# Performance work log

Hardware: AMD Instinct MI355X
Metric: run time of the kernel (lower is better)

The kernel has to match this reference:

```python
import jax, jax.numpy as jnp
import numpy as np

N, E, G = 50000, 800000, 200
F_IN, C, HEADS = 16, 64, 4
HID = C * HEADS  # 256


def setup_inputs() -> dict:
    key = jax.random.key(0)
    ks = jax.random.split(key, 30)
    rn = lambda k, s, sc=0.1: jax.random.normal(k, s, jnp.float32) * sc
    inp = {
        'x': jax.random.normal(ks[0], (N, F_IN), jnp.float32),
        'edge_index': jax.random.randint(ks[1], (2, E), 0, N, jnp.int32),
        'batch': jnp.sort(jax.random.randint(ks[2], (N,), 0, G, jnp.int32)),
        'Wl1': rn(ks[3], (F_IN, HID)), 'Wr1': rn(ks[4], (F_IN, HID)),
        'att1': rn(ks[5], (HEADS, C)), 'b1': rn(ks[6], (HID,)),
        'g1': jnp.ones((HID,), jnp.float32), 'be1': jnp.zeros((HID,), jnp.float32),
        'Wl2': rn(ks[7], (HID, HID)), 'Wr2': rn(ks[8], (HID, HID)),
        'att2': rn(ks[9], (HEADS, C)), 'b2': rn(ks[10], (HID,)),
        'g2': jnp.ones((HID,), jnp.float32), 'be2': jnp.zeros((HID,), jnp.float32),
        # GATv2 layer 3: 256 -> 64, 1 head, mean (concat=False)
        'Wl3': rn(ks[11], (HID, C)), 'Wr3': rn(ks[12], (HID, C)),
        'att3': rn(ks[13], (1, C)), 'b3': rn(ks[14], (C,)),
        'g3': jnp.ones((C,), jnp.float32), 'be3': jnp.zeros((C,), jnp.float32),
        # classifier MLP: 128 -> 64 -> 1
        'Wc1': rn(ks[15], (2 * C, C)), 'bc1': rn(ks[16], (C,)),
        'Wc2': rn(ks[17], (C, 1)), 'bc2': rn(ks[18], (1,)),
    }
    return inp


def _gatv2(x, src, dst, Wl, Wr, att, b, heads, c, concat):
    n = x.shape[0]
    xl = (x @ Wl).reshape(n, heads, c)
    xr = (x @ Wr).reshape(n, heads, c)
    s = jax.nn.leaky_relu(xl[src] + xr[dst], 0.2)       # [E', H, C]
    e = jnp.einsum('ehc,hc->eh', s, att)                 # [E', H]
    m = jax.ops.segment_max(e, dst, num_segments=n)
    p = jnp.exp(e - m[dst])
    denom = jax.ops.segment_sum(p, dst, num_segments=n)
    alpha = p / (denom[dst] + 1e-16)
    out = jax.ops.segment_sum(alpha[:, :, None] * xl[src], dst, num_segments=n)
    out = out.reshape(n, heads * c) if concat else out.mean(axis=1)
    return out + b


def _bn(x, g, b):
    mu = x.mean(0)
    v = x.var(0)
    return (x - mu) * jax.lax.rsqrt(v + 1e-5) * g + b


def reference(x, edge_index, batch,
              Wl1, Wr1, att1, b1, g1, be1,
              Wl2, Wr2, att2, b2, g2, be2,
              Wl3, Wr3, att3, b3, g3, be3,
              Wc1, bc1, Wc2, bc2):
    n = x.shape[0]
    loop = jnp.arange(n, dtype=edge_index.dtype)
    src = jnp.concatenate([edge_index[0], loop])  # PyG add_self_loops=True
    dst = jnp.concatenate([edge_index[1], loop])

    h = _gatv2(x, src, dst, Wl1, Wr1, att1, b1, HEADS, C, True)
    h = jax.nn.elu(_bn(h, g1, be1))  # dropout disabled (eval)
    h = _gatv2(h, src, dst, Wl2, Wr2, att2, b2, HEADS, C, True)
    h = jax.nn.elu(_bn(h, g2, be2))
    h = _gatv2(h, src, dst, Wl3, Wr3, att3, b3, 1, C, False)
    h = _bn(h, g3, be3)

    cnt = jax.ops.segment_sum(jnp.ones((n, 1), h.dtype), batch, num_segments=G)
    mean_pool = jax.ops.segment_sum(h, batch, num_segments=G) / jnp.maximum(cnt, 1.0)
    max_pool = jax.ops.segment_max(h, batch, num_segments=G)
    pooled = jnp.concatenate([mean_pool, max_pool], axis=1)  # [G, 128]

    out = jax.nn.relu(pooled @ Wc1 + bc1)
    out = out @ Wc2 + bc2  # [G, 1]
    return out
```

## Files before the change

### kernel.cpp

```cpp
#include <hip/hip_runtime.h>
#include <math.h>

#define N_NODES 50000
#define N_EDGES 800000
#define ET (N_EDGES + N_NODES)
#define N_GRAPHS 200
#define F_INN 16
#define C_DIM 64
#define N_HEADS 4
#define HIDD 256
#define SCAN_BLOCKS ((N_NODES + 255) / 256)

typedef __attribute__((ext_vector_type(8))) short short8;
typedef __attribute__((ext_vector_type(8))) ushort ushort8;
typedef __attribute__((ext_vector_type(4))) float f32x4;
typedef __attribute__((ext_vector_type(2))) float f32x2;

#define LOG2E 1.44269504088896340736f

__device__ __forceinline__ float bf2f(ushort u) {
  return __uint_as_float(((unsigned)u) << 16);
}
__device__ __forceinline__ ushort f2bf(float f) {
  unsigned u = __float_as_uint(f);
  u += 0x7fff + ((u >> 16) & 1);
  return (ushort)(u >> 16);
}
__device__ __forceinline__ float ex2(float x) {
#if __has_builtin(__builtin_amdgcn_exp2f)
  return __builtin_amdgcn_exp2f(x);
#else
  return exp2f(x);
#endif
}

__device__ __forceinline__ f32x2 emax2(f32x2 a, f32x2 b) {
#if __has_builtin(__builtin_elementwise_max)
  return __builtin_elementwise_max(a, b);
#else
  f32x2 r;
  r.x = fmaxf(a.x, b.x);
  r.y = fmaxf(a.y, b.y);
  return r;
#endif
}

template<int K, int M>
__global__ __launch_bounds__(256) void gemm_dual(
    const float* __restrict__ A, const float* __restrict__ Bl,
    const float* __restrict__ Br, ushort* __restrict__ Clb,
    ushort* __restrict__ Crb, int nrows)
{
  __shared__ __align__(16) float As[16][64];
  __shared__ __align__(16) float Bls[16][64];
  __shared__ __align__(16) float Brs[16][64];
  int tid = threadIdx.x;
  int row0 = blockIdx.x * 64;
  int col0 = blockIdx.y * 64;
  int tr = (tid >> 4) << 2;
  int tc = (tid & 15) << 2;
  float accL[4][4] = {{0.f}}, accR[4][4] = {{0.f}};
  int arow = tid >> 2, ak = (tid & 3) << 2;
  int brow = tid >> 4, bcol = (tid & 15) << 2;
  for (int k0 = 0; k0 < K; k0 += 16) {
    float4 av = make_float4(0.f, 0.f, 0.f, 0.f);
    int gr = row0 + arow;
    if (gr < nrows) av = *(const float4*)&A[(size_t)gr * K + k0 + ak];
    As[ak + 0][arow] = av.x;
    As[ak + 1][arow] = av.y;
    As[ak + 2][arow] = av.z;
    As[ak + 3][arow] = av.w;
    *(float4*)&Bls[brow][bcol] = *(const float4*)&Bl[(size_t)(k0 + brow) * M + col0 + bcol];
    *(float4*)&Brs[brow][bcol] = *(const float4*)&Br[(size_t)(k0 + brow) * M + col0 + bcol];
    __syncthreads();
    #pragma unroll
    for (int k = 0; k < 16; ++k) {
      float4 a = *(const float4*)&As[k][tr];
      float4 bl = *(const float4*)&Bls[k][tc];
      float4 br = *(const float4*)&Brs[k][tc];
      float aa[4] = {a.x, a.y, a.z, a.w};
      float lb[4] = {bl.x, bl.y, bl.z, bl.w};
      float rb[4] = {br.x, br.y, br.z, br.w};
      #pragma unroll
      for (int ii = 0; ii < 4; ++ii)
        #pragma unroll
        for (int jj = 0; jj < 4; ++jj) {
          accL[ii][jj] = fmaf(aa[ii], lb[jj], accL[ii][jj]);
          accR[ii][jj] = fmaf(aa[ii], rb[jj], accR[ii][jj]);
        }
    }
    __syncthreads();
  }
  #pragma unroll
  for (int ii = 0; ii < 4; ++ii) {
    int gr = row0 + tr + ii;
    if (gr < nrows) {
      *(ushort4*)&Clb[(size_t)gr * M + col0 + tc] =
          make_ushort4(f2bf(accL[ii][0]), f2bf(accL[ii][1]),
                       f2bf(accL[ii][2]), f2bf(accL[ii][3]));
      *(ushort4*)&Crb[(size_t)gr * M + col0 + tc] =
          make_ushort4(f2bf(accR[ii][0]), f2bf(accR[ii][1]),
                       f2bf(accR[ii][2]), f2bf(accR[ii][3]));
    }
  }
}

__device__ __forceinline__ void split_bf16(float a, ushort& hi, ushort& lo) {
  unsigned u = __float_as_uint(a);
  hi = (ushort)(u >> 16);
  float ah = __uint_as_float(u & 0xffff0000u);
  float r = a - ah;
  lo = (ushort)(__float_as_uint(r) >> 16);
}

template<int K, int N>
__global__ void convertB(const float* __restrict__ W, ushort* __restrict__ BTmat) {
  int idx = blockIdx.x * blockDim.x + threadIdx.x;
  if (idx >= K * N) return;
  int k = idx / N, n = idx - k * N;
  ushort hi, lo;
  split_bf16(W[idx], hi, lo);
  size_t dst = ((size_t)(k >> 3) * N + n) * 8 + (k & 7);
  BTmat[dst] = hi;
  BTmat[(size_t)(K / 8) * N * 8 + dst] = lo;
}

template<int N>
__global__ __launch_bounds__(N * 2) void gemm_fused(
    const float* __restrict__ H, const float* __restrict__ gsum,
    const float* __restrict__ gsumsq, const float* __restrict__ g,
    const float* __restrict__ be, const ushort* __restrict__ BT,
    ushort* __restrict__ Clb, ushort* __restrict__ Crb)
{
  constexpr int THREADS = N * 2;
  constexpr int PLANE = 32 * N * 8;
  __shared__ float SCs[256], SHs[256];
  __shared__ ushort Ah_s[32 * 256];
  __shared__ ushort Al_s[32 * 256];
  const int tid = threadIdx.x;
  const int brow0 = blockIdx.x * 32;

  const float invn = 1.0f / (float)N_NODES;
  for (int c = tid; c < 256; c += THREADS) {
    float mu = gsum[c] * invn;
    float var = gsumsq[c] * invn - mu * mu;
    float sc = g[c] * rsqrtf(var + 1e-5f);
    SCs[c] = sc;
    SHs[c] = be[c] - mu * sc;
  }
  __syncthreads();

  for (int gid = tid; gid < 1024; gid += THREADS) {
    int r = gid >> 5;
    int ch0 = (gid & 31) * 8;
    int grow = min(brow0 + r, N_NODES - 1);
    float4 v0 = *(const float4*)&H[(size_t)grow * 256 + ch0];
    float4 v1 = *(const float4*)&H[(size_t)grow * 256 + ch0 + 4];
    float4 sc0 = *(const float4*)&SCs[ch0];
    float4 sc1 = *(const float4*)&SCs[ch0 + 4];
    float4 sh0 = *(const float4*)&SHs[ch0];
    float4 sh1 = *(const float4*)&SHs[ch0 + 4];
    float vv[8] = {v0.x, v0.y, v0.z, v0.w, v1.x, v1.y, v1.z, v1.w};
    float scv[8] = {sc0.x, sc0.y, sc0.z, sc0.w, sc1.x, sc1.y, sc1.z, sc1.w};
    float shv[8] = {sh0.x, sh0.y, sh0.z, sh0.w, sh1.x, sh1.y, sh1.z, sh1.w};
    short8 hi8, lo8;
    #pragma unroll
    for (int j = 0; j < 8; ++j) {
      float t = fmaf(vv[j], scv[j], shv[j]);
      float e = t > 0.f ? t : __expf(t) - 1.f;
      ushort h, l;
      split_bf16(e, h, l);
      hi8[j] = (short)h;
      lo8[j] = (short)l;
    }
    int off = r * 512 + ((ch0 * 2) ^ ((r & 7) << 4));
    *(short8*)((char*)Ah_s + off) = hi8;
    *(short8*)((char*)Al_s + off) = lo8;
  }
  __syncthreads();

  const int wave = tid >> 6, lane = tid & 63;
  const int cn = lane & 15, kgrp = lane >> 4;
  const int combc = wave * 64;
  const bool isR = combc >= N;
  const ushort* Bh = BT + (isR ? 2 * PLANE : 0);
  const ushort* Bl_ = Bh + PLANE;
  const int cb = combc & (N - 1);
  f32x4 acc[2][4];
  #pragma unroll
  for (int rt = 0; rt < 2; ++rt)
    #pragma unroll
    for (int ct = 0; ct < 4; ++ct) acc[rt][ct] = (f32x4)(0.f);

  #pragma unroll 2
  for (int k0 = 0; k0 < 256; k0 += 32) {
    short8 ah[2], al[2];
    #pragma unroll
    for (int rt = 0; rt < 2; ++rt) {
      int row = rt * 16 + cn;
      int off = row * 512 + (((k0 * 2) + kgrp * 16) ^ ((row & 7) << 4));
      ah[rt] = *(const short8*)((const char*)Ah_s + off);
      al[rt] = *(const short8*)((const char*)Al_s + off);
    }
    const size_t bbase = (size_t)((k0 >> 3) + kgrp) * (N * 8);
    #pragma unroll
    for (int ct = 0; ct < 4; ++ct) {
      const size_t bo = bbase + (size_t)(cb + ct * 16 + cn) * 8;
      short8 bh = *(const short8*)&Bh[bo];
      short8 bl = *(const short8*)&Bl_[bo];
      #pragma unroll
      for (int rt = 0; rt < 2; ++rt) {
        acc[rt][ct] = __builtin_amdgcn_mfma_f32_16x16x32_bf16(ah[rt], bh, acc[rt][ct], 0, 0, 0);
        acc[rt][ct] = __builtin_amdgcn_mfma_f32_16x16x32_bf16(ah[rt], bl, acc[rt][ct], 0, 0, 0);
        acc[rt][ct] = __builtin_amdgcn_mfma_f32_16x16x32_bf16(al[rt], bh, acc[rt][ct], 0, 0, 0);
      }
    }
  }

  #pragma unroll
  for (int ct = 0; ct < 4; ++ct) {
    int cc = cb + ct * 16 + cn;
    #pragma unroll
    for (int rt = 0; rt < 2; ++rt) {
      int crow0 = brow0 + rt * 16 + kgrp * 4;
      #pragma unroll
      for (int j = 0; j < 4; ++j) {
        int rr = crow0 + j;
        if (rr < N_NODES) {
          if (!isR) Clb[(size_t)rr * N + cc] = f2bf(acc[rt][ct][j]);
          else      Crb[(size_t)rr * N + cc] = f2bf(acc[rt][ct][j]);
        }
      }
    }
  }
}

__global__ void hist_kernel(const int* __restrict__ dsts, int* __restrict__ curs) {
  int i = blockIdx.x * blockDim.x + threadIdx.x;
  if (i >= ET) return;
  int d = (i < N_EDGES) ? dsts[i] : i - N_EDGES;
  atomicAdd(&curs[d], 1);
}

__global__ __launch_bounds__(256) void scan_part(
    const int* __restrict__ curs, int* __restrict__ rows, int* __restrict__ bsum)
{
  __shared__ int tmp[256];
  int t = threadIdx.x;
  int i = blockIdx.x * 256 + t;
  int v = (i < N_NODES) ? curs[i] : 0;
  tmp[t] = v;
  __syncthreads();
  #pragma unroll
  for (int off = 1; off < 256; off <<= 1) {
    int u = (t >= off) ? tmp[t - off] : 0;
    __syncthreads();
    tmp[t] += u;
    __syncthreads();
  }
  if (i < N_NODES) rows[i] = tmp[t] - v;
  if (t == 255) bsum[blockIdx.x] = tmp[255];
}

__global__ __launch_bounds__(256) void scan_bsums(
    const int* __restrict__ bsum, int* __restrict__ boff)
{
  __shared__ int tmp[256];
  int t = threadIdx.x;
  int v = (t < SCAN_BLOCKS) ? bsum[t] : 0;
  tmp[t] = v;
  __syncthreads();
  #pragma unroll
  for (int off = 1; off < 256; off <<= 1) {
    int u = (t >= off) ? tmp[t - off] : 0;
    __syncthreads();
    tmp[t] += u;
    __syncthreads();
  }
  if (t < SCAN_BLOCKS) boff[t] = tmp[t] - v;
}

__global__ __launch_bounds__(256) void scan_apply(
    int* __restrict__ rows, const int* __restrict__ boff, int* __restrict__ curs)
{
  int i = blockIdx.x * 256 + threadIdx.x;
  if (i < N_NODES) {
    int r = rows[i] + boff[blockIdx.x];
    rows[i] = r;
    curs[i] = r;
  }
  if (i == 0) rows[N_NODES] = ET;
}

__global__ void scatter_kernel(const int* __restrict__ srcs, const int* __restrict__ dsts,
                               int* __restrict__ curs, int* __restrict__ esrc) {
  int i = blockIdx.x * blockDim.x + threadIdx.x;
  if (i >= ET) return;
  int s, d;
  if (i < N_EDGES) { s = srcs[i]; d = dsts[i]; } else { s = d = i - N_EDGES; }
  int pos = atomicAdd(&curs[d], 1);
  esrc[pos] = s;
}

__global__ __launch_bounds__(256) void flash256(
    const ushort* __restrict__ xl, const ushort* __restrict__ xr,
    const float* __restrict__ att, const int* __restrict__ rows,
    const int* __restrict__ esrc, float* __restrict__ out)
{
  const int wave = threadIdx.x >> 6, lane = threadIdx.x & 63;
  const int d = blockIdx.x * 4 + wave;
  const unsigned lo4 = lane * 4;
  int beg = rows[d], end = rows[d + 1];
  ushort4 ur = *(const ushort4*)&xr[(size_t)d * 256 + lo4];
  float xq0 = bf2f(ur.x), xq1 = bf2f(ur.y), xq2 = bf2f(ur.z), xq3 = bf2f(ur.w);
  float4 w = *(const float4*)&att[lo4];
  w.x *= LOG2E; w.y *= LOG2E; w.z *= LOG2E; w.w *= LOG2E;
  auto score = [&](float b0, float b1, float b2, float b3) {
    float v0 = b0 + xq0, v1 = b1 + xq1, v2 = b2 + xq2, v3 = b3 + xq3;
    v0 = v0 > 0.f ? v0 : 0.2f * v0;
    v1 = v1 > 0.f ? v1 : 0.2f * v1;
    v2 = v2 > 0.f ? v2 : 0.2f * v2;
    v3 = v3 > 0.f ? v3 : 0.2f * v3;
    return fmaf(v0, w.x, fmaf(v1, w.y, fmaf(v2, w.z, v3 * w.w)));
  };
  float m = -INFINITY, s = 0.f;
  float a0 = 0.f, a1 = 0.f, a2 = 0.f, a3 = 0.f;
  int p = beg;
  for (; p + 4 <= end; p += 4) {
    int s1 = esrc[p], s2 = esrc[p + 1], s3 = esrc[p + 2], s4 = esrc[p + 3];
    unsigned o1 = ((unsigned)s1 << 8) + lo4;
    unsigned o2 = ((unsigned)s2 << 8) + lo4;
    unsigned o3 = ((unsigned)s3 << 8) + lo4;
    unsigned o4 = ((unsigned)s4 << 8) + lo4;
    ushort4 u1 = *(const ushort4*)&xl[o1];
    ushort4 u2 = *(const ushort4*)&xl[o2];
    ushort4 u3 = *(const ushort4*)&xl[o3];
    ushort4 u4 = *(const ushort4*)&xl[o4];
    float b10 = bf2f(u1.x), b11 = bf2f(u1.y), b12 = bf2f(u1.z), b13 = bf2f(u1.w);
    float b20 = bf2f(u2.x), b21 = bf2f(u2.y), b22 = bf2f(u2.z), b23 = bf2f(u2.w);
    float b30 = bf2f(u3.x), b31 = bf2f(u3.y), b32 = bf2f(u3.z), b33 = bf2f(u3.w);
    float b40 = bf2f(u4.x), b41 = bf2f(u4.y), b42 = bf2f(u4.z), b43 = bf2f(u4.w);
    float e1 = score(b10, b11, b12, b13);
    float e2 = score(b20, b21, b22, b23);
    float e3 = score(b30, b31, b32, b33);
    float e4 = score(b40, b41, b42, b43);
    e1 += __shfl_xor(e1, 1); e2 += __shfl_xor(e2, 1);
    e3 += __shfl_xor(e3, 1); e4 += __shfl_xor(e4, 1);
    e1 += __shfl_xor(e1, 2); e2 += __shfl_xor(e2, 2);
    e3 += __shfl_xor(e3, 2); e4 += __shfl_xor(e4, 2);
    e1 += __shfl_xor(e1, 4); e2 += __shfl_xor(e2, 4);
    e3 += __shfl_xor(e3, 4); e4 += __shfl_xor(e4, 4);
    e1 += __shfl_xor(e1, 8); e2 += __shfl_xor(e2, 8);
    e3 += __shfl_xor(e3, 8); e4 += __shfl_xor(e4, 8);
    float gm = fmaxf(fmaxf(e1, e2), fmaxf(e3, e4));
    if (__all(gm <= m + 8.0f)) {
      float p1 = ex2(e1 - m);
      float p2 = ex2(e2 - m);
      float p3 = ex2(e3 - m);
      float p4 = ex2(e4 - m);
      s += (p1 + p2) + (p3 + p4);
      a0 = fmaf(p1, b10, fmaf(p2, b20, fmaf(p3, b30, fmaf(p4, b40, a0))));
      a1 = fmaf(p1, b11, fmaf(p2, b21, fmaf(p3, b31, fmaf(p4, b41, a1))));
      a2 = fmaf(p1, b12, fmaf(p2, b22, fmaf(p3, b32, fmaf(p4, b42, a2))));
      a3 = fmaf(p1, b13, fmaf(p2, b23, fmaf(p3, b33, fmaf(p4, b43, a3))));
    } else {
      float mn = fmaxf(m, gm);
      float f = ex2(m - mn);
      float p1 = ex2(e1 - mn);
      float p2 = ex2(e2 - mn);
      float p3 = ex2(e3 - mn);
      float p4 = ex2(e4 - mn);
      s = s * f + ((p1 + p2) + (p3 + p4));
      a0 = fmaf(a0, f, fmaf(p1, b10, fmaf(p2, b20, fmaf(p3, b30, p4 * b40))));
      a1 = fmaf(a1, f, fmaf(p1, b11, fmaf(p2, b21, fmaf(p3, b31, p4 * b41))));
      a2 = fmaf(a2, f, fmaf(p1, b12, fmaf(p2, b22, fmaf(p3, b32, p4 * b42))));
      a3 = fmaf(a3, f, fmaf(p1, b13, fmaf(p2, b23, fmaf(p3, b33, p4 * b43))));
      m = mn;
    }
  }
  for (; p < end; ++p) {
    int s1 = esrc[p];
    unsigned o1 = ((unsigned)s1 << 8) + lo4;
    ushort4 u1 = *(const ushort4*)&xl[o1];
    float b10 = bf2f(u1.x), b11 = bf2f(u1.y), b12 = bf2f(u1.z), b13 = bf2f(u1.w);
    float e1 = score(b10, b11, b12, b13);
    e1 += __shfl_xor(e1, 1);
    e1 += __shfl_xor(e1, 2);
    e1 += __shfl_xor(e1, 4);
    e1 += __shfl_xor(e1, 8);
    float mn = fmaxf(m, e1);
    float f = ex2(m - mn);
    float p1 = ex2(e1 - mn);
    s = fmaf(s, f, p1);
    a0 = fmaf(a0, f, p1 * b10);
    a1 = fmaf(a1, f, p1 * b11);
    a2 = fmaf(a2, f, p1 * b12);
    a3 = fmaf(a3, f, p1 * b13);
    m = mn;
  }
  float inv = 1.f / (s + 1e-16f);
  *(float4*)&out[(size_t)d * 256 + lo4] =
      make_float4(a0 * inv, a1 * inv, a2 * inv, a3 * inv);
}

__global__ __launch_bounds__(256) void flash64(
    const ushort* __restrict__ xl, const ushort* __restrict__ xr,
    const float* __restrict__ att, const int* __restrict__ rows,
    const int* __restrict__ esrc, float* __restrict__ out)
{
  const int wave = threadIdx.x >> 6, lane = threadIdx.x & 63;
  const int di = lane >> 3, sl = lane & 7;
  const int idx = blockIdx.x * 32 + wave * 8 + di;
  const bool valid = idx < N_NODES;
  const int d = valid ? idx : N_NODES - 1;
  const unsigned ch = sl * 8;
  ushort8 uxr = *(const ushort8*)&xr[(size_t)d * 64 + ch];
  float4 wa = *(const float4*)&att[ch];
  float4 wb = *(const float4*)&att[ch + 4];
  f32x2 xr0 = {bf2f(uxr[0]), bf2f(uxr[1])}, xr1 = {bf2f(uxr[2]), bf2f(uxr[3])};
  f32x2 xr2 = {bf2f(uxr[4]), bf2f(uxr[5])}, xr3 = {bf2f(uxr[6]), bf2f(uxr[7])};
  f32x2 w0 = {wa.x * LOG2E, wa.y * LOG2E}, w1 = {wa.z * LOG2E, wa.w * LOG2E};
  f32x2 w2 = {wb.x * LOG2E, wb.y * LOG2E}, w3 = {wb.z * LOG2E, wb.w * LOG2E};
  int beg = rows[d], end = rows[d + 1];
  float m = -INFINITY, s = 0.f;
  f32x2 a0 = {0.f, 0.f}, a1 = {0.f, 0.f}, a2 = {0.f, 0.f}, a3 = {0.f, 0.f};

  auto loadb = [&](int src, f32x2 b[4]) {
    unsigned off = ((unsigned)src << 6) + ch;
    ushort8 u = *(const ushort8*)&xl[off];
    b[0] = f32x2{bf2f(u[0]), bf2f(u[1])};
    b[1] = f32x2{bf2f(u[2]), bf2f(u[3])};
    b[2] = f32x2{bf2f(u[4]), bf2f(u[5])};
    b[3] = f32x2{bf2f(u[6]), bf2f(u[7])};
  };
  auto scoreP = [&](const f32x2 b[4]) -> float {
    f32x2 v0 = b[0] + xr0, v1 = b[1] + xr1, v2 = b[2] + xr2, v3 = b[3] + xr3;
    v0 = emax2(v0, v0 * 0.2f);
    v1 = emax2(v1, v1 * 0.2f);
    v2 = emax2(v2, v2 * 0.2f);
    v3 = emax2(v3, v3 * 0.2f);
    f32x2 dd = (v0 * w0 + v1 * w1) + (v2 * w2 + v3 * w3);
    return dd.x + dd.y;
  };
  auto one_edge = [&](int src) {
    f32x2 b[4];
    loadb(src, b);
    float e = scoreP(b);
    e += __shfl_xor(e, 1);
    e += __shfl_xor(e, 2);
    e += __shfl_xor(e, 4);
    float mn = fmaxf(m, e);
    float f = ex2(m - mn);
    float pe = ex2(e - mn);
    s = s * f + pe;
    a0 = a0 * f + b[0] * pe;
    a1 = a1 * f + b[1] * pe;
    a2 = a2 * f + b[2] * pe;
    a3 = a3 * f + b[3] * pe;
    m = mn;
  };

  int p = beg;
  int hd = min(end, (beg + 3) & ~3);
  for (; p < hd; ++p) one_edge(esrc[p]);
  for (; p + 4 <= end; p += 4) {
    int4 sv = *(const int4*)&esrc[p];
    f32x2 b1[4], b2[4], b3[4], b4[4];
    loadb(sv.x, b1);
    loadb(sv.y, b2);
    loadb(sv.z, b3);
    loadb(sv.w, b4);
    float e1 = scoreP(b1);
    float e2 = scoreP(b2);
    float e3 = scoreP(b3);
    float e4 = scoreP(b4);
    e1 += __shfl_xor(e1, 1); e2 += __shfl_xor(e2, 1);
    e3 += __shfl_xor(e3, 1); e4 += __shfl_xor(e4, 1);
    e1 += __shfl_xor(e1, 2); e2 += __shfl_xor(e2, 2);
    e3 += __shfl_xor(e3, 2); e4 += __shfl_xor(e4, 2);
    e1 += __shfl_xor(e1, 4); e2 += __shfl_xor(e2, 4);
    e3 += __shfl_xor(e3, 4); e4 += __shfl_xor(e4, 4);
    float gm = fmaxf(fmaxf(e1, e2), fmaxf(e3, e4));
    if (__all(gm <= m + 8.0f)) {
      float p1 = ex2(e1 - m);
      float p2 = ex2(e2 - m);
      float p3 = ex2(e3 - m);
      float p4 = ex2(e4 - m);
      s += (p1 + p2) + (p3 + p4);
      a0 = a0 + ((b1[0] * p1 + b2[0] * p2) + (b3[0] * p3 + b4[0] * p4));
      a1 = a1 + ((b1[1] * p1 + b2[1] * p2) + (b3[1] * p3 + b4[1] * p4));
      a2 = a2 + ((b1[2] * p1 + b2[2] * p2) + (b3[2] * p3 + b4[2] * p4));
      a3 = a3 + ((b1[3] * p1 + b2[3] * p2) + (b3[3] * p3 + b4[3] * p4));
    } else {
      float mn = fmaxf(m, gm);
      float f = ex2(m - mn);
      float p1 = ex2(e1 - mn);
      float p2 = ex2(e2 - mn);
      float p3 = ex2(e3 - mn);
      float p4 = ex2(e4 - mn);
      s = s * f + ((p1 + p2) + (p3 + p4));
      a0 = a0 * f + ((b1[0] * p1 + b2[0] * p2) + (b3[0] * p3 + b4[0] * p4));
      a1 = a1 * f + ((b1[1] * p1 + b2[1] * p2) + (b3[1] * p3 + b4[1] * p4));
      a2 = a2 * f + ((b1[2] * p1 + b2[2] * p2) + (b3[2] * p3 + b4[2] * p4));
      a3 = a3 * f + ((b1[3] * p1 + b2[3] * p2) + (b3[3] * p3 + b4[3] * p4));
      m = mn;
    }
  }
  for (; p < end; ++p) one_edge(esrc[p]);

  if (valid) {
    float inv = 1.f / (s + 1e-16f);
    *(float4*)&out[(size_t)d * 64 + ch] =
        make_float4(a0.x * inv, a0.y * inv, a1.x * inv, a1.y * inv);
    *(float4*)&out[(size_t)d * 64 + ch + 4] =
        make_float4(a2.x * inv, a2.y * inv, a3.x * inv, a3.y * inv);
  }
}

template<int D_, int RPB>
__global__ __launch_bounds__(256) void bn_stats(const float* __restrict__ h,
    float* __restrict__ gsum, float* __restrict__ gsumsq, int nrows)
{
  constexpr int RG = 256 / D_;
  int c = threadIdx.x % D_;
  int rg = threadIdx.x / D_;
  int r0 = blockIdx.x * RPB;
  float s = 0.f, sq = 0.f;
  int rend = min(r0 + RPB, nrows);
  for (int r = r0 + rg; r < rend; r += RG) {
    float v = h[(size_t)r * D_ + c];
    s += v;
    sq = fmaf(v, v, sq);
  }
  atomicAdd(&gsum[c], s);
  atomicAdd(&gsumsq[c], sq);
}

__global__ __launch_bounds__(256) void pool_mlp(
    const float* __restrict__ h3, const int* __restrict__ batch,
    const float* __restrict__ gsum, const float* __restrict__ gsumsq,
    const float* __restrict__ g3, const float* __restrict__ be3,
    const float* __restrict__ Wc1, const float* __restrict__ bc1,
    const float* __restrict__ Wc2, const float* __restrict__ bc2,
    float* __restrict__ outp)
{
  int g = blockIdx.x;
  int t = threadIdx.x;
  int lane = t & 63, w = t >> 6;
  int lo, hi;
  {
    int a = 0, b = N_NODES;
    while (a < b) { int mid = (a + b) >> 1; if (batch[mid] < g) a = mid + 1; else b = mid; }
    lo = a;
    b = N_NODES;
    while (a < b) { int mid = (a + b) >> 1; if (batch[mid] < g + 1) a = mid + 1; else b = mid; }
    hi = a;
  }
  const float invn = 1.0f / (float)N_NODES;
  float mu = gsum[lane] * invn;
  float var = gsumsq[lane] * invn - mu * mu;
  float scl = g3[lane] * rsqrtf(var + 1e-5f);
  float shf = be3[lane] - mu * scl;
  float s = 0.f, mx = -INFINITY;
  for (int r = lo + w; r < hi; r += 4) {
    float v = fmaf(h3[(size_t)r * 64 + lane], scl, shf);
    s += v;
    mx = fmaxf(mx, v);
  }
  __shared__ float ssum[4][64];
  __shared__ float smax[4][64];
  __shared__ float pooled[128];
  ssum[w][lane] = s;
  smax[w][lane] = mx;
  __syncthreads();
  if (w == 0) {
    float tot = ssum[0][lane] + ssum[1][lane] + ssum[2][lane] + ssum[3][lane];
    float m4 = fmaxf(fmaxf(smax[0][lane], smax[1][lane]),
                     fmaxf(smax[2][lane], smax[3][lane]));
    float cnt = (float)(hi - lo);
    pooled[lane] = tot / fmaxf(cnt, 1.f);
    pooled[64 + lane] = m4;
  }
  __syncthreads();
  if (w == 0) {
    float a = bc1[lane];
    #pragma unroll 8
    for (int k = 0; k < 128; ++k) a = fmaf(pooled[k], Wc1[k * 64 + lane], a);
    a = fmaxf(a, 0.f);
    float v = a * Wc2[lane];
    v += __shfl_xor(v, 1);
    v += __shfl_xor(v, 2);
    v += __shfl_xor(v, 4);
    v += __shfl_xor(v, 8);
    v += __shfl_xor(v, 16);
    v += __shfl_xor(v, 32);
    if (lane == 0) outp[g] = v + bc2[0];
  }
}

extern "C" void kernel_launch(void* const* d_in, const int* in_sizes, int n_in,
                              void* d_out, int out_size, void* d_ws, size_t ws_size,
                              hipStream_t stream)
{
  const float* x    = (const float*)d_in[0];
  const int*   ei   = (const int*)d_in[1];
  const int*   batch= (const int*)d_in[2];
  const float* Wl1  = (const float*)d_in[3];
  const float* Wr1  = (const float*)d_in[4];
  const float* att1 = (const float*)d_in[5];
  const float* g1   = (const float*)d_in[7];
  const float* be1  = (const float*)d_in[8];
  const float* Wl2  = (const float*)d_in[9];
  const float* Wr2  = (const float*)d_in[10];
  const float* att2 = (const float*)d_in[11];
  const float* g2   = (const float*)d_in[13];
  const float* be2  = (const float*)d_in[14];
  const float* Wl3  = (const float*)d_in[15];
  const float* Wr3  = (const float*)d_in[16];
  const float* att3 = (const float*)d_in[17];
  const float* g3   = (const float*)d_in[19];
  const float* be3  = (const float*)d_in[20];
  const float* Wc1  = (const float*)d_in[21];
  const float* bc1  = (const float*)d_in[22];
  const float* Wc2  = (const float*)d_in[23];
  const float* bc2  = (const float*)d_in[24];

  const int* srcs = ei;
  const int* dsts = ei + N_EDGES;

  float* ws = (float*)d_ws;
  size_t o = 0;
  ushort* XLB = (ushort*)(ws + o); o += (size_t)N_NODES * HIDD / 2;
  ushort* XRB = (ushort*)(ws + o); o += (size_t)N_NODES * HIDD / 2;
  float* Hb = ws + o;            o += (size_t)N_NODES * HIDD;
  ushort* BT2 = (ushort*)(ws + o); o += (size_t)4 * 32 * 256 * 8 / 2;
  ushort* BT3 = (ushort*)(ws + o); o += (size_t)4 * 32 * 64 * 8 / 2;
  int* ESRC = (int*)(ws + o);    o += ET;
  int* ROWS = (int*)(ws + o);    o += N_NODES + 1;
  int* CURS = (int*)(ws + o);    o += N_NODES;
  int* BSUM = (int*)(ws + o);    o += SCAN_BLOCKS;
  int* BOFF = (int*)(ws + o);    o += SCAN_BLOCKS;
  float* GS  = ws + o;           o += 256;
  float* GSQ = ws + o;           o += 256;

  const int ROW_BLOCKS = (N_NODES + 63) / 64;
  const int ROW_BLOCKS32 = (N_NODES + 31) / 32;
  const int DST_BLOCKS = (N_NODES + 3) / 4;
  constexpr int PLANE2 = 32 * 256 * 8;
  constexpr int PLANE3 = 32 * 64 * 8;

  convertB<256, 256><<<(65536 + 255) / 256, 256, 0, stream>>>(Wl2, BT2);
  convertB<256, 256><<<(65536 + 255) / 256, 256, 0, stream>>>(Wr2, BT2 + 2 * PLANE2);
  convertB<256, 64><<<(16384 + 255) / 256, 256, 0, stream>>>(Wl3, BT3);
  convertB<256, 64><<<(16384 + 255) / 256, 256, 0, stream>>>(Wr3, BT3 + 2 * PLANE3);

  hipMemsetAsync(CURS, 0, N_NODES * 4, stream);
  hist_kernel<<<(ET + 255) / 256, 256, 0, stream>>>(dsts, CURS);
  scan_part<<<SCAN_BLOCKS, 256, 0, stream>>>(CURS, ROWS, BSUM);
  scan_bsums<<<1, 256, 0, stream>>>(BSUM, BOFF);
  scan_apply<<<SCAN_BLOCKS, 256, 0, stream>>>(ROWS, BOFF, CURS);
  scatter_kernel<<<(ET + 255) / 256, 256, 0, stream>>>(srcs, dsts, CURS, ESRC);

  gemm_dual<16, 256><<<dim3(ROW_BLOCKS, 4), 256, 0, stream>>>(
      x, Wl1, Wr1, XLB, XRB, N_NODES);
  flash256<<<DST_BLOCKS, 256, 0, stream>>>(XLB, XRB, att1, ROWS, ESRC, Hb);
  hipMemsetAsync(GS, 0, 512 * 4, stream);
  bn_stats<256, 64><<<ROW_BLOCKS, 256, 0, stream>>>(Hb, GS, GSQ, N_NODES);

  gemm_fused<256><<<ROW_BLOCKS32, 512, 0, stream>>>(
      Hb, GS, GSQ, g1, be1, BT2, XLB, XRB);
  flash256<<<DST_BLOCKS, 256, 0, stream>>>(XLB, XRB, att2, ROWS, ESRC, Hb);
  hipMemsetAsync(GS, 0, 512 * 4, stream);
  bn_stats<256, 64><<<ROW_BLOCKS, 256, 0, stream>>>(Hb, GS, GSQ, N_NODES);

  gemm_fused<64><<<ROW_BLOCKS32, 128, 0, stream>>>(
      Hb, GS, GSQ, g2, be2, BT3, XLB, XRB);
  flash64<<<(N_NODES + 31) / 32, 256, 0, stream>>>(XLB, XRB, att3, ROWS, ESRC, Hb);
  hipMemsetAsync(GS, 0, 512 * 4, stream);
  bn_stats<64, 256><<<(N_NODES + 255) / 256, 256, 0, stream>>>(Hb, GS, GSQ, N_NODES);

  pool_mlp<<<N_GRAPHS, 256, 0, stream>>>(Hb, batch, GS, GSQ, g3, be3,
                                         Wc1, bc1, Wc2, bc2, (float*)d_out);
}
```

Baseline: 542.6 us.

## Store projected features as fp16 and use packed fp16 math with dot2 in aggregation

The GEMM outputs xl/xr are now stored as fp16 instead of bf16. The edge attention kernels compute the leaky-relu score with packed half2 add and max, and use v_dot2 for both the attention dot product and the alpha-weighted accumulation. Byte permutes pair up features across edges for the dot2 accumulation. This removes the per-element bf16-to-fp32 unpacking and halves the VALU op count in the gather loops. The cost is fp16 range and precision risk: intermediate scores and probabilities are rounded toward zero into half, and large activations could overflow.

```diff
diff --git a/kernel.cpp b/kernel.cpp
--- a/kernel.cpp
+++ b/kernel.cpp
@@ -15,17 +15,10 @@
 typedef __attribute__((ext_vector_type(8))) ushort ushort8;
 typedef __attribute__((ext_vector_type(4))) float f32x4;
 typedef __attribute__((ext_vector_type(2))) float f32x2;
+typedef __attribute__((ext_vector_type(2))) _Float16 h16x2;
 
 #define LOG2E 1.44269504088896340736f
 
-__device__ __forceinline__ float bf2f(ushort u) {
-  return __uint_as_float(((unsigned)u) << 16);
-}
-__device__ __forceinline__ ushort f2bf(float f) {
-  unsigned u = __float_as_uint(f);
-  u += 0x7fff + ((u >> 16) & 1);
-  return (ushort)(u >> 16);
-}
 __device__ __forceinline__ float ex2(float x) {
 #if __has_builtin(__builtin_amdgcn_exp2f)
   return __builtin_amdgcn_exp2f(x);
@@ -34,16 +27,57 @@
 #endif
 }
 
-__device__ __forceinline__ f32x2 emax2(f32x2 a, f32x2 b) {
+__device__ __forceinline__ h16x2 bc16(unsigned u) {
+  union { unsigned u; h16x2 h; } c; c.u = u; return c.h;
+}
+__device__ __forceinline__ ushort f2h(float f) {
+  union { _Float16 h; ushort u; } c; c.h = (_Float16)f; return c.u;
+}
+
+#if __has_builtin(__builtin_amdgcn_cvt_pkrtz)
+using hw2 = decltype(__builtin_amdgcn_cvt_pkrtz(0.f, 0.f));
+__device__ __forceinline__ h16x2 pkrtz(float a, float b) {
+  union { hw2 w; h16x2 h; } c;
+  c.w = __builtin_amdgcn_cvt_pkrtz(a, b);
+  return c.h;
+}
+#else
+__device__ __forceinline__ h16x2 pkrtz(float a, float b) {
+  h16x2 r; r[0] = (_Float16)a; r[1] = (_Float16)b; return r;
+}
+#endif
+
+__device__ __forceinline__ float fdot2f(h16x2 a, h16x2 b, float c) {
+#if __has_builtin(__builtin_amdgcn_fdot2) && __has_builtin(__builtin_amdgcn_cvt_pkrtz)
+  union { h16x2 h; hw2 w; } ca, cb;
+  ca.h = a; cb.h = b;
+  return __builtin_amdgcn_fdot2(ca.w, cb.w, c, false);
+#else
+  return (float)a[0] * (float)b[0] + (float)a[1] * (float)b[1] + c;
+#endif
+}
+__device__ __forceinline__ h16x2 hmax2(h16x2 a, h16x2 b) {
 #if __has_builtin(__builtin_elementwise_max)
   return __builtin_elementwise_max(a, b);
 #else
-  f32x2 r;
-  r.x = fmaxf(a.x, b.x);
-  r.y = fmaxf(a.y, b.y);
+  h16x2 r; r[0] = a[0] > b[0] ? a[0] : b[0]; r[1] = a[1] > b[1] ? a[1] : b[1]; return r;
+#endif
+}
+__device__ __forceinline__ unsigned permu(unsigned s0, unsigned s1, unsigned sel) {
+#if __has_builtin(__builtin_amdgcn_perm)
+  return __builtin_amdgcn_perm(s0, s1, sel);
+#else
+  unsigned long long cat = (((unsigned long long)s0) << 32) | s1;
+  unsigned r = 0;
+  for (int i = 0; i < 4; ++i) {
+    unsigned b = (sel >> (8 * i)) & 0xff;
+    r |= ((unsigned)((cat >> (8 * (b & 7))) & 0xff)) << (8 * i);
+  }
   return r;
 #endif
 }
+#define PAIR_LO(A, B) permu((B), (A), 0x05040100u)
+#define PAIR_HI(A, B) permu((B), (A), 0x07060302u)
 
 template<int K, int M>
 __global__ __launch_bounds__(256) void gemm_dual(
@@ -96,11 +130,11 @@
     int gr = row0 + tr + ii;
     if (gr < nrows) {
       *(ushort4*)&Clb[(size_t)gr * M + col0 + tc] =
-          make_ushort4(f2bf(accL[ii][0]), f2bf(accL[ii][1]),
-                       f2bf(accL[ii][2]), f2bf(accL[ii][3]));
+          make_ushort4(f2h(accL[ii][0]), f2h(accL[ii][1]),
+                       f2h(accL[ii][2]), f2h(accL[ii][3]));
       *(ushort4*)&Crb[(size_t)gr * M + col0 + tc] =
-          make_ushort4(f2bf(accR[ii][0]), f2bf(accR[ii][1]),
-                       f2bf(accR[ii][2]), f2bf(accR[ii][3]));
+          make_ushort4(f2h(accR[ii][0]), f2h(accR[ii][1]),
+                       f2h(accR[ii][2]), f2h(accR[ii][3]));
     }
   }
 }
@@ -227,8 +261,8 @@
       for (int j = 0; j < 4; ++j) {
         int rr = crow0 + j;
         if (rr < N_NODES) {
-          if (!isR) Clb[(size_t)rr * N + cc] = f2bf(acc[rt][ct][j]);
-          else      Crb[(size_t)rr * N + cc] = f2bf(acc[rt][ct][j]);
+          if (!isR) Clb[(size_t)rr * N + cc] = f2h(acc[rt][ct][j]);
+          else      Crb[(size_t)rr * N + cc] = f2h(acc[rt][ct][j]);
         }
       }
     }
@@ -311,39 +345,33 @@
   const int d = blockIdx.x * 4 + wave;
   const unsigned lo4 = lane * 4;
   int beg = rows[d], end = rows[d + 1];
-  ushort4 ur = *(const ushort4*)&xr[(size_t)d * 256 + lo4];
-  float xq0 = bf2f(ur.x), xq1 = bf2f(ur.y), xq2 = bf2f(ur.z), xq3 = bf2f(ur.w);
+  uint2 urx = *(const uint2*)&xr[(size_t)d * 256 + lo4];
+  h16x2 x01 = bc16(urx.x), x23 = bc16(urx.y);
   float4 w = *(const float4*)&att[lo4];
-  w.x *= LOG2E; w.y *= LOG2E; w.z *= LOG2E; w.w *= LOG2E;
-  auto score = [&](float b0, float b1, float b2, float b3) {
-    float v0 = b0 + xq0, v1 = b1 + xq1, v2 = b2 + xq2, v3 = b3 + xq3;
-    v0 = v0 > 0.f ? v0 : 0.2f * v0;
-    v1 = v1 > 0.f ? v1 : 0.2f * v1;
-    v2 = v2 > 0.f ? v2 : 0.2f * v2;
-    v3 = v3 > 0.f ? v3 : 0.2f * v3;
-    return fmaf(v0, w.x, fmaf(v1, w.y, fmaf(v2, w.z, v3 * w.w)));
+  h16x2 w01 = pkrtz(w.x * LOG2E, w.y * LOG2E);
+  h16x2 w23 = pkrtz(w.z * LOG2E, w.w * LOG2E);
+  const _Float16 c2 = (_Float16)0.2f;
+  const h16x2 c02 = {c2, c2};
+  auto score = [&](uint2 u) -> float {
+    h16x2 v01 = bc16(u.x) + x01;
+    h16x2 v23 = bc16(u.y) + x23;
+    v01 = hmax2(v01, v01 * c02);
+    v23 = hmax2(v23, v23 * c02);
+    return fdot2f(v01, w01, fdot2f(v23, w23, 0.f));
   };
   float m = -INFINITY, s = 0.f;
   float a0 = 0.f, a1 = 0.f, a2 = 0.f, a3 = 0.f;
   int p = beg;
   for (; p + 4 <= end; p += 4) {
     int s1 = esrc[p], s2 = esrc[p + 1], s3 = esrc[p + 2], s4 = esrc[p + 3];
-    unsigned o1 = ((unsigned)s1 << 8) + lo4;
-    unsigned o2 = ((unsigned)s2 << 8) + lo4;
-    unsigned o3 = ((unsigned)s3 << 8) + lo4;
-    unsigned o4 = ((unsigned)s4 << 8) + lo4;
-    ushort4 u1 = *(const ushort4*)&xl[o1];
-    ushort4 u2 = *(const ushort4*)&xl[o2];
-    ushort4 u3 = *(const ushort4*)&xl[o3];
-    ushort4 u4 = *(const ushort4*)&xl[o4];
-    float b10 = bf2f(u1.x), b11 = bf2f(u1.y), b12 = bf2f(u1.z), b13 = bf2f(u1.w);
-    float b20 = bf2f(u2.x), b21 = bf2f(u2.y), b22 = bf2f(u2.z), b23 = bf2f(u2.w);
-    float b30 = bf2f(u3.x), b31 = bf2f(u3.y), b32 = bf2f(u3.z), b33 = bf2f(u3.w);
-    float b40 = bf2f(u4.x), b41 = bf2f(u4.y), b42 = bf2f(u4.z), b43 = bf2f(u4.w);
-    float e1 = score(b10, b11, b12, b13);
-    float e2 = score(b20, b21, b22, b23);
-    float e3 = score(b30, b31, b32, b33);
-    float e4 = score(b40, b41, b42, b43);
+    uint2 u1 = *(const uint2*)&xl[((unsigned)s1 << 8) + lo4];
+    uint2 u2 = *(const uint2*)&xl[((unsigned)s2 << 8) + lo4];
+    uint2 u3 = *(const uint2*)&xl[((unsigned)s3 << 8) + lo4];
+    uint2 u4 = *(const uint2*)&xl[((unsigned)s4 << 8) + lo4];
+    float e1 = score(u1);
+    float e2 = score(u2);
+    float e3 = score(u3);
+    float e4 = score(u4);
     e1 += __shfl_xor(e1, 1); e2 += __shfl_xor(e2, 1);
     e3 += __shfl_xor(e3, 1); e4 += __shfl_xor(e4, 1);
     e1 += __shfl_xor(e1, 2); e2 += __shfl_xor(e2, 2);
@@ -353,37 +381,37 @@
     e1 += __shfl_xor(e1, 8); e2 += __shfl_xor(e2, 8);
     e3 += __shfl_xor(e3, 8); e4 += __shfl_xor(e4, 8);
     float gm = fmaxf(fmaxf(e1, e2), fmaxf(e3, e4));
+    float p1, p2, p3, p4;
     if (__all(gm <= m + 8.0f)) {
-      float p1 = ex2(e1 - m);
-      float p2 = ex2(e2 - m);
-      float p3 = ex2(e3 - m);
-      float p4 = ex2(e4 - m);
-      s += (p1 + p2) + (p3 + p4);
-      a0 = fmaf(p1, b10, fmaf(p2, b20, fmaf(p3, b30, fmaf(p4, b40, a0))));
-      a1 = fmaf(p1, b11, fmaf(p2, b21, fmaf(p3, b31, fmaf(p4, b41, a1))));
-      a2 = fmaf(p1, b12, fmaf(p2, b22, fmaf(p3, b32, fmaf(p4, b42, a2))));
-      a3 = fmaf(p1, b13, fmaf(p2, b23, fmaf(p3, b33, fmaf(p4, b43, a3))));
+      p1 = ex2(e1 - m);
+      p2 = ex2(e2 - m);
+      p3 = ex2(e3 - m);
+      p4 = ex2(e4 - m);
     } else {
       float mn = fmaxf(m, gm);
       float f = ex2(m - mn);
-      float p1 = ex2(e1 - mn);
-      float p2 = ex2(e2 - mn);
-      float p3 = ex2(e3 - mn);
-      float p4 = ex2(e4 - mn);
-      s = s * f + ((p1 + p2) + (p3 + p4));
-      a0 = fmaf(a0, f, fmaf(p1, b10, fmaf(p2, b20, fmaf(p3, b30, p4 * b40))));
-      a1 = fmaf(a1, f, fmaf(p1, b11, fmaf(p2, b21, fmaf(p3, b31, p4 * b41))));
-      a2 = fmaf(a2, f, fmaf(p1, b12, fmaf(p2, b22, fmaf(p3, b32, p4 * b42))));
-      a3 = fmaf(a3, f, fmaf(p1, b13, fmaf(p2, b23, fmaf(p3, b33, p4 * b43))));
+      p1 = ex2(e1 - mn);
+      p2 = ex2(e2 - mn);
+      p3 = ex2(e3 - mn);
+      p4 = ex2(e4 - mn);
+      s *= f; a0 *= f; a1 *= f; a2 *= f; a3 *= f;
       m = mn;
     }
+    s += (p1 + p2) + (p3 + p4);
+    h16x2 p12 = pkrtz(p1, p2), p34 = pkrtz(p3, p4);
+    a0 = fdot2f(p12, bc16(PAIR_LO(u1.x, u2.x)), a0);
+    a0 = fdot2f(p34, bc16(PAIR_LO(u3.x, u4.x)), a0);
+    a1 = fdot2f(p12, bc16(PAIR_HI(u1.x, u2.x)), a1);
+    a1 = fdot2f(p34, bc16(PAIR_HI(u3.x, u4.x)), a1);
+    a2 = fdot2f(p12, bc16(PAIR_LO(u1.y, u2.y)), a2);
+    a2 = fdot2f(p34, bc16(PAIR_LO(u3.y, u4.y)), a2);
+    a3 = fdot2f(p12, bc16(PAIR_HI(u1.y, u2.y)), a3);
+    a3 = fdot2f(p34, bc16(PAIR_HI(u3.y, u4.y)), a3);
   }
   for (; p < end; ++p) {
     int s1 = esrc[p];
-    unsigned o1 = ((unsigned)s1 << 8) + lo4;
-    ushort4 u1 = *(const ushort4*)&xl[o1];
-    float b10 = bf2f(u1.x), b11 = bf2f(u1.y), b12 = bf2f(u1.z), b13 = bf2f(u1.w);
-    float e1 = score(b10, b11, b12, b13);
+    uint2 u1 = *(const uint2*)&xl[((unsigned)s1 << 8) + lo4];
+    float e1 = score(u1);
     e1 += __shfl_xor(e1, 1);
     e1 += __shfl_xor(e1, 2);
     e1 += __shfl_xor(e1, 4);
@@ -391,11 +419,12 @@
     float mn = fmaxf(m, e1);
     float f = ex2(m - mn);
     float p1 = ex2(e1 - mn);
+    h16x2 b01 = bc16(u1.x), b23 = bc16(u1.y);
     s = fmaf(s, f, p1);
-    a0 = fmaf(a0, f, p1 * b10);
-    a1 = fmaf(a1, f, p1 * b11);
-    a2 = fmaf(a2, f, p1 * b12);
-    a3 = fmaf(a3, f, p1 * b13);
+    a0 = fmaf(a0, f, p1 * (float)b01[0]);
+    a1 = fmaf(a1, f, p1 * (float)b01[1]);
+    a2 = fmaf(a2, f, p1 * (float)b23[0]);
+    a3 = fmaf(a3, f, p1 * (float)b23[1]);
     m = mn;
   }
   float inv = 1.f / (s + 1e-16f);
@@ -414,49 +443,51 @@
   const bool valid = idx < N_NODES;
   const int d = valid ? idx : N_NODES - 1;
   const unsigned ch = sl * 8;
-  ushort8 uxr = *(const ushort8*)&xr[(size_t)d * 64 + ch];
+  uint4 uxr = *(const uint4*)&xr[(size_t)d * 64 + ch];
   float4 wa = *(const float4*)&att[ch];
   float4 wb = *(const float4*)&att[ch + 4];
-  f32x2 xr0 = {bf2f(uxr[0]), bf2f(uxr[1])}, xr1 = {bf2f(uxr[2]), bf2f(uxr[3])};
-  f32x2 xr2 = {bf2f(uxr[4]), bf2f(uxr[5])}, xr3 = {bf2f(uxr[6]), bf2f(uxr[7])};
-  f32x2 w0 = {wa.x * LOG2E, wa.y * LOG2E}, w1 = {wa.z * LOG2E, wa.w * LOG2E};
-  f32x2 w2 = {wb.x * LOG2E, wb.y * LOG2E}, w3 = {wb.z * LOG2E, wb.w * LOG2E};
+  h16x2 x0 = bc16(uxr.x), x1 = bc16(uxr.y), x2 = bc16(uxr.z), x3 = bc16(uxr.w);
+  h16x2 w0 = pkrtz(wa.x * LOG2E, wa.y * LOG2E);
+  h16x2 w1 = pkrtz(wa.z * LOG2E, wa.w * LOG2E);
+  h16x2 w2 = pkrtz(wb.x * LOG2E, wb.y * LOG2E);
+  h16x2 w3 = pkrtz(wb.z * LOG2E, wb.w * LOG2E);
+  const _Float16 c2 = (_Float16)0.2f;
+  const h16x2 c02 = {c2, c2};
   int beg = rows[d], end = rows[d + 1];
   float m = -INFINITY, s = 0.f;
-  f32x2 a0 = {0.f, 0.f}, a1 = {0.f, 0.f}, a2 = {0.f, 0.f}, a3 = {0.f, 0.f};
-
-  auto loadb = [&](int src, f32x2 b[4]) {
-    unsigned off = ((unsigned)src << 6) + ch;
-    ushort8 u = *(const ushort8*)&xl[off];
-    b[0] = f32x2{bf2f(u[0]), bf2f(u[1])};
-    b[1] = f32x2{bf2f(u[2]), bf2f(u[3])};
-    b[2] = f32x2{bf2f(u[4]), bf2f(u[5])};
-    b[3] = f32x2{bf2f(u[6]), bf2f(u[7])};
-  };
-  auto scoreP = [&](const f32x2 b[4]) -> float {
-    f32x2 v0 = b[0] + xr0, v1 = b[1] + xr1, v2 = b[2] + xr2, v3 = b[3] + xr3;
-    v0 = emax2(v0, v0 * 0.2f);
-    v1 = emax2(v1, v1 * 0.2f);
-    v2 = emax2(v2, v2 * 0.2f);
-    v3 = emax2(v3, v3 * 0.2f);
-    f32x2 dd = (v0 * w0 + v1 * w1) + (v2 * w2 + v3 * w3);
-    return dd.x + dd.y;
+  float a0 = 0.f, a1 = 0.f, a2 = 0.f, a3 = 0.f;
+  float a4 = 0.f, a5 = 0.f, a6 = 0.f, a7 = 0.f;
+
+  auto score = [&](uint4 u) -> float {
+    h16x2 v0 = bc16(u.x) + x0;
+    h16x2 v1 = bc16(u.y) + x1;
+    h16x2 v2 = bc16(u.z) + x2;
+    h16x2 v3 = bc16(u.w) + x3;
+    v0 = hmax2(v0, v0 * c02);
+    v1 = hmax2(v1, v1 * c02);
+    v2 = hmax2(v2, v2 * c02);
+    v3 = hmax2(v3, v3 * c02);
+    return fdot2f(v0, w0, fdot2f(v1, w1, fdot2f(v2, w2, fdot2f(v3, w3, 0.f))));
   };
   auto one_edge = [&](int src) {
-    f32x2 b[4];
-    loadb(src, b);
-    float e = scoreP(b);
+    uint4 u = *(const uint4*)&xl[((unsigned)src << 6) + ch];
+    float e = score(u);
     e += __shfl_xor(e, 1);
     e += __shfl_xor(e, 2);
     e += __shfl_xor(e, 4);
     float mn = fmaxf(m, e);
     float f = ex2(m - mn);
     float pe = ex2(e - mn);
+    h16x2 b0 = bc16(u.x), b1 = bc16(u.y), b2 = bc16(u.z), b3 = bc16(u.w);
     s = s * f + pe;
-    a0 = a0 * f + b[0] * pe;
-    a1 = a1 * f + b[1] * pe;
-    a2 = a2 * f + b[2] * pe;
-    a3 = a3 * f + b[3] * pe;
+    a0 = fmaf(a0, f, pe * (float)b0[0]);
+    a1 = fmaf(a1, f, pe * (float)b0[1]);
+    a2 = fmaf(a2, f, pe * (float)b1[0]);
+    a3 = fmaf(a3, f, pe * (float)b1[1]);
+    a4 = fmaf(a4, f, pe * (float)b2[0]);
+    a5 = fmaf(a5, f, pe * (float)b2[1]);
+    a6 = fmaf(a6, f, pe * (float)b3[0]);
+    a7 = fmaf(a7, f, pe * (float)b3[1]);
     m = mn;
   };
 
@@ -465,15 +496,14 @@
   for (; p < hd; ++p) one_edge(esrc[p]);
   for (; p + 4 <= end; p += 4) {
     int4 sv = *(const int4*)&esrc[p];
-    f32x2 b1[4], b2[4], b3[4], b4[4];
-    loadb(sv.x, b1);
-    loadb(sv.y, b2);
-    loadb(sv.z, b3);
-    loadb(sv.w, b4);
-    float e1 = scoreP(b1);
-    float e2 = scoreP(b2);
-    float e3 = scoreP(b3);
-    float e4 = scoreP(b4);
+    uint4 u1 = *(const uint4*)&xl[((unsigned)sv.x << 6) + ch];
+    uint4 u2 = *(const uint4*)&xl[((unsigned)sv.y << 6) + ch];
+    uint4 u3 = *(const uint4*)&xl[((unsigned)sv.z << 6) + ch];
+    uint4 u4 = *(const uint4*)&xl[((unsigned)sv.w << 6) + ch];
+    float e1 = score(u1);
+    float e2 = score(u2);
+    float e3 = score(u3);
+    float e4 = score(u4);
     e1 += __shfl_xor(e1, 1); e2 += __shfl_xor(e2, 1);
     e3 += __shfl_xor(e3, 1); e4 += __shfl_xor(e4, 1);
     e1 += __shfl_xor(e1, 2); e2 += __shfl_xor(e2, 2);
@@ -481,39 +511,51 @@
     e1 += __shfl_xor(e1, 4); e2 += __shfl_xor(e2, 4);
     e3 += __shfl_xor(e3, 4); e4 += __shfl_xor(e4, 4);
     float gm = fmaxf(fmaxf(e1, e2), fmaxf(e3, e4));
+    float p1, p2, p3, p4;
     if (__all(gm <= m + 8.0f)) {
-      float p1 = ex2(e1 - m);
-      float p2 = ex2(e2 - m);
-      float p3 = ex2(e3 - m);
-      float p4 = ex2(e4 - m);
-      s += (p1 + p2) + (p3 + p4);
-      a0 = a0 + ((b1[0] * p1 + b2[0] * p2) + (b3[0] * p3 + b4[0] * p4));
-      a1 = a1 + ((b1[1] * p1 + b2[1] * p2) + (b3[1] * p3 + b4[1] * p4));
-      a2 = a2 + ((b1[2] * p1 + b2[2] * p2) + (b3[2] * p3 + b4[2] * p4));
-      a3 = a3 + ((b1[3] * p1 + b2[3] * p2) + (b3[3] * p3 + b4[3] * p4));
+      p1 = ex2(e1 - m);
+      p2 = ex2(e2 - m);
+      p3 = ex2(e3 - m);
+      p4 = ex2(e4 - m);
     } else {
       float mn = fmaxf(m, gm);
       float f = ex2(m - mn);
-      float p1 = ex2(e1 - mn);
-      float p2 = ex2(e2 - mn);
-      float p3 = ex2(e3 - mn);
-      float p4 = ex2(e4 - mn);
-      s = s * f + ((p1 + p2) + (p3 + p4));
-      a0 = a0 * f + ((b1[0] * p1 + b2[0] * p2) + (b3[0] * p3 + b4[0] * p4));
-      a1 = a1 * f + ((b1[1] * p1 + b2[1] * p2) + (b3[1] * p3 + b4[1] * p4));
-      a2 = a2 * f + ((b1[2] * p1 + b2[2] * p2) + (b3[2] * p3 + b4[2] * p4));
-      a3 = a3 * f + ((b1[3] * p1 + b2[3] * p2) + (b3[3] * p3 + b4[3] * p4));
+      p1 = ex2(e1 - mn);
+      p2 = ex2(e2 - mn);
+      p3 = ex2(e3 - mn);
+      p4 = ex2(e4 - mn);
+      s *= f;
+      a0 *= f; a1 *= f; a2 *= f; a3 *= f;
+      a4 *= f; a5 *= f; a6 *= f; a7 *= f;
       m = mn;
     }
+    s += (p1 + p2) + (p3 + p4);
+    h16x2 p12 = pkrtz(p1, p2), p34 = pkrtz(p3, p4);
+    a0 = fdot2f(p12, bc16(PAIR_LO(u1.x, u2.x)), a0);
+    a0 = fdot2f(p34, bc16(PAIR_LO(u3.x, u4.x)), a0);
+    a1 = fdot2f(p12, bc16(PAIR_HI(u1.x, u2.x)), a1);
+    a1 = fdot2f(p34, bc16(PAIR_HI(u3.x, u4.x)), a1);
+    a2 = fdot2f(p12, bc16(PAIR_LO(u1.y, u2.y)), a2);
+    a2 = fdot2f(p34, bc16(PAIR_LO(u3.y, u4.y)), a2);
+    a3 = fdot2f(p12, bc16(PAIR_HI(u1.y, u2.y)), a3);
+    a3 = fdot2f(p34, bc16(PAIR_HI(u3.y, u4.y)), a3);
+    a4 = fdot2f(p12, bc16(PAIR_LO(u1.z, u2.z)), a4);
+    a4 = fdot2f(p34, bc16(PAIR_LO(u3.z, u4.z)), a4);
+    a5 = fdot2f(p12, bc16(PAIR_HI(u1.z, u2.z)), a5);
+    a5 = fdot2f(p34, bc16(PAIR_HI(u3.z, u4.z)), a5);
+    a6 = fdot2f(p12, bc16(PAIR_LO(u1.w, u2.w)), a6);
+    a6 = fdot2f(p34, bc16(PAIR_LO(u3.w, u4.w)), a6);
+    a7 = fdot2f(p12, bc16(PAIR_HI(u1.w, u2.w)), a7);
+    a7 = fdot2f(p34, bc16(PAIR_HI(u3.w, u4.w)), a7);
   }
   for (; p < end; ++p) one_edge(esrc[p]);
 
   if (valid) {
     float inv = 1.f / (s + 1e-16f);
     *(float4*)&out[(size_t)d * 64 + ch] =
-        make_float4(a0.x * inv, a0.y * inv, a1.x * inv, a1.y * inv);
+        make_float4(a0 * inv, a1 * inv, a2 * inv, a3 * inv);
     *(float4*)&out[(size_t)d * 64 + ch + 4] =
-        make_float4(a2.x * inv, a2.y * inv, a3.x * inv, a3.y * inv);
+        make_float4(a4 * inv, a5 * inv, a6 * inv, a7 * inv);
   }
 }
 
```

Result: faster. 530.5 us (-2.2%).
